# Kernel optimization log

Hardware: AMD Instinct MI355X
Metric: run time of the kernel (lower is better)

## Reference

```python
import jax, jax.numpy as jnp
import numpy as np

B, NW, L, D = 32, 64, 49, 192
HEADS, PROJ = 8, 256
HD = PROJ // HEADS  # 32


def setup_inputs() -> dict:
    key = jax.random.key(0)
    ks = jax.random.split(key, 12)
    s = 0.02
    return {
        "query": jax.random.normal(ks[0], (B, NW, L, D), jnp.float32),
        "key_": jax.random.normal(ks[1], (B, NW, L, D), jnp.float32),
        "value": jax.random.normal(ks[2], (B, NW, L, D), jnp.float32),
        "mask": jax.random.randint(ks[3], (1, NW, 1, L, L), 0, 2).astype(bool),
        "Wq": jax.random.normal(ks[4], (D, PROJ), jnp.float32) * s,
        "bq": jnp.zeros((PROJ,), jnp.float32),
        "Wk": jax.random.normal(ks[5], (D, PROJ), jnp.float32) * s,
        "bk": jnp.zeros((PROJ,), jnp.float32),
        "Wv": jax.random.normal(ks[6], (D, PROJ), jnp.float32) * s,
        "Ww": jax.random.normal(ks[7], (PROJ, D), jnp.float32) * s,
        "bw": jnp.zeros((D,), jnp.float32),
    }


def reference(query, key_, value, mask, Wq, bq, Wk, bk, Wv, Ww, bw):
    scale = 1.0 / (HD ** 0.5)
    # projections, split heads: [B, NW, L, PROJ] -> [B, NW, H, L, HD]
    def split_heads(x):
        return x.reshape(B, NW, L, HEADS, HD).transpose(0, 1, 3, 2, 4)

    q = split_heads(query @ Wq + bq)
    k = split_heads(key_ @ Wk + bk)
    v = split_heads(value @ Wv)  # no bias, matching proj_v

    # scores: [B, NW, H, L, L]
    scores = jnp.einsum("bwhnc,bwhmc->bwhnm", q, k) * scale
    scores = jnp.where(mask, jnp.float32(-1000.0), scores)
    attn = jax.nn.softmax(scores, axis=-1)
    # dropout inactive: training=False and enable_sampling=False

    out = jnp.einsum("bwhnm,bwhmc->bwhnc", attn, v)
    out = out.transpose(0, 1, 3, 2, 4).reshape(B, NW, L, PROJ)
    out = out @ Ww + bw
    return out
```

## Files before the change

### kernel.cpp

```cpp
#include <hip/hip_runtime.h>

#define B_    32
#define NW_   64
#define BW_   2048
#define L_    49
#define D_    192
#define PROJ_ 256
#define H_    8
#define HD_   32

typedef __attribute__((ext_vector_type(8))) short bf16x8;
typedef __attribute__((ext_vector_type(4))) float f32x4;

#define XB_OFF    0
#define QKP_OFF   25600
#define VT_OFF    91136
#define LDS_BYTES 123904

__device__ __forceinline__ short f2bf(float f) {
    union { float f; unsigned u; } v; v.f = f;
    unsigned r = v.u + 0x7FFFu + ((v.u >> 16) & 1u);
    return (short)(r >> 16);
}

__global__ __launch_bounds__(256) void prep_weights(
    const float* __restrict__ Wq, const float* __restrict__ Wk,
    const float* __restrict__ Wv, const float* __restrict__ Ww,
    short* __restrict__ Wqt, short* __restrict__ Wkt,
    short* __restrict__ Wvt, short* __restrict__ Wwt)
{
    const int sel = blockIdx.y;
    const int n   = blockIdx.x;
    const int tid = threadIdx.x;
    if (sel < 3) {
        const float* src = (sel == 0) ? Wq : (sel == 1) ? Wk : Wv;
        short* dst = (sel == 0) ? Wqt : (sel == 1) ? Wkt : Wvt;
        if (tid < D_) dst[n * D_ + tid] = f2bf(src[tid * PROJ_ + n]);
    } else {
        if (n < D_) Wwt[n * PROJ_ + tid] = f2bf(Ww[tid * D_ + n]);
    }
}

__global__ __launch_bounds__(256) void prep_mask(
    const int* __restrict__ mask, unsigned long long* __restrict__ mbits)
{
    const int w    = blockIdx.x;
    const int wave = threadIdx.x >> 6;
    const int lane = threadIdx.x & 63;
    for (int qq = 0; qq < 16; ++qq) {
        const int q = wave * 16 + qq;
        int val = 0;
        if (q < L_ && lane < L_) val = mask[w * (L_ * L_) + q * L_ + lane];
        unsigned long long bits = __ballot(val != 0);
        if (lane == 0) mbits[w * 64 + q] = bits;
    }
}

__global__ __launch_bounds__(512) void fused_kernel(
    const float* __restrict__ query, const float* __restrict__ key_,
    const float* __restrict__ value,
    const short* __restrict__ Wqt, const short* __restrict__ Wkt,
    const short* __restrict__ Wvt,
    const float* __restrict__ bq, const float* __restrict__ bk,
    const unsigned long long* __restrict__ mbits,
    const short* __restrict__ Wwt, const float* __restrict__ bwb,
    float* __restrict__ out)
{
    extern __shared__ char lds[];
    short* Xb = (short*)(lds + XB_OFF);

    const int bw   = blockIdx.x;
    const int w    = bw & (NW_ - 1);
    const int tid  = threadIdx.x;
    const int wave = tid >> 6;
    const int lane = tid & 63;
    const int m16  = lane & 15;
    const int quad = lane >> 4;

    const int swz2 = ((m16 >> 1) & 3) << 4;
    const int swz3 = (m16 & 7) << 4;

    char* myQKP = lds + QKP_OFF + wave * 8192;
    char* myVT  = lds + VT_OFF  + wave * 4096;

    #pragma unroll
    for (int sel = 0; sel < 3; ++sel) {
        const float* x  = (sel == 0) ? query : (sel == 1) ? key_ : value;
        const short* Wt = (sel == 0) ? Wqt : (sel == 1) ? Wkt : Wvt;

        __syncthreads();
        #pragma unroll
        for (int it = 0; it < 6; ++it) {
            const int i = tid + it * 512;
            const int l = i / 48, c4 = i - l * 48;
            short4 s4 = {0, 0, 0, 0};
            if (l < L_) {
                float4 v = *(const float4*)&x[((size_t)bw * L_ + l) * D_ + c4 * 4];
                s4.x = f2bf(v.x); s4.y = f2bf(v.y); s4.z = f2bf(v.z); s4.w = f2bf(v.w);
            }
            *(short4*)&Xb[l * 200 + c4 * 4] = s4;
        }
        __syncthreads();

        f32x4 acc[4][2];
        #pragma unroll
        for (int mt = 0; mt < 4; ++mt)
            #pragma unroll
            for (int nt = 0; nt < 2; ++nt)
                acc[mt][nt] = (f32x4){0.f, 0.f, 0.f, 0.f};

        #pragma unroll
        for (int kc = 0; kc < 6; ++kc) {
            bf16x8 af[4], bf[2];
            #pragma unroll
            for (int mt = 0; mt < 4; ++mt)
                af[mt] = *(const bf16x8*)&Xb[(mt * 16 + m16) * 200 + kc * 32 + quad * 8];
            #pragma unroll
            for (int nt = 0; nt < 2; ++nt)
                bf[nt] = *(const bf16x8*)&Wt[(size_t)(wave * 32 + nt * 16 + m16) * D_ + kc * 32 + quad * 8];
            #pragma unroll
            for (int mt = 0; mt < 4; ++mt)
                #pragma unroll
                for (int nt = 0; nt < 2; ++nt)
                    acc[mt][nt] = __builtin_amdgcn_mfma_f32_16x16x32_bf16(
                        af[mt], bf[nt], acc[mt][nt], 0, 0, 0);
        }

        if (sel < 2) {
            char* dstb = myQKP + sel * 4096;
            #pragma unroll
            for (int nt = 0; nt < 2; ++nt) {
                const int c = nt * 16 + m16;
                const float bias = ((sel == 0) ? bq : bk)[wave * 32 + c];
                #pragma unroll
                for (int mt = 0; mt < 4; ++mt)
                    #pragma unroll
                    for (int r = 0; r < 4; ++r) {
                        const int i = mt * 16 + quad * 4 + r;
                        *(short*)(dstb + i * 64 + ((2 * c) ^ (((i >> 1) & 3) << 4))) =
                            f2bf(acc[mt][nt][r] + bias);
                    }
            }
        } else {
            #pragma unroll
            for (int nt = 0; nt < 2; ++nt) {
                const int c = nt * 16 + m16;
                #pragma unroll
                for (int mt = 0; mt < 4; ++mt) {
                    short4 o4;
                    o4.x = f2bf(acc[mt][nt][0]); o4.y = f2bf(acc[mt][nt][1]);
                    o4.z = f2bf(acc[mt][nt][2]); o4.w = f2bf(acc[mt][nt][3]);
                    *(short4*)(myVT + c * 128 + ((mt * 32 + quad * 8) ^ swz3)) = o4;
                }
            }
        }
    }

    unsigned long long mb[4];
    #pragma unroll
    for (int nt = 0; nt < 4; ++nt) mb[nt] = mbits[w * 64 + nt * 16 + m16];

    const float scale = 0.17677669529663687f;

    f32x4 sacc[4][4];
    #pragma unroll
    for (int mt = 0; mt < 4; ++mt)
        #pragma unroll
        for (int nt = 0; nt < 4; ++nt)
            sacc[mt][nt] = (f32x4){0.f, 0.f, 0.f, 0.f};
    {
        bf16x8 kf[4], qf[4];
        #pragma unroll
        for (int mt = 0; mt < 4; ++mt)
            kf[mt] = *(const bf16x8*)(myQKP + 4096 + (mt * 16 + m16) * 64 + ((quad * 16) ^ swz2));
        #pragma unroll
        for (int nt = 0; nt < 4; ++nt)
            qf[nt] = *(const bf16x8*)(myQKP + (nt * 16 + m16) * 64 + ((quad * 16) ^ swz2));
        #pragma unroll
        for (int mt = 0; mt < 4; ++mt)
            #pragma unroll
            for (int nt = 0; nt < 4; ++nt)
                sacc[mt][nt] = __builtin_amdgcn_mfma_f32_16x16x32_bf16(
                    kf[mt], qf[nt], sacc[mt][nt], 0, 0, 0);
    }

    #pragma unroll
    for (int nt = 0; nt < 4; ++nt) {
        float e[4][4];
        float mx = -1e30f;
        #pragma unroll
        for (int mt = 0; mt < 4; ++mt)
            #pragma unroll
            for (int r = 0; r < 4; ++r) {
                const int k = mt * 16 + quad * 4 + r;
                float v = sacc[mt][nt][r] * scale;
                if (k >= L_) v = -INFINITY;
                else if ((mb[nt] >> k) & 1ull) v = -1000.0f;
                e[mt][r] = v;
                mx = fmaxf(mx, v);
            }
        mx = fmaxf(mx, __shfl_xor(mx, 16, 64));
        mx = fmaxf(mx, __shfl_xor(mx, 32, 64));
        float sum = 0.f;
        #pragma unroll
        for (int mt = 0; mt < 4; ++mt)
            #pragma unroll
            for (int r = 0; r < 4; ++r) {
                const float ev = __expf(e[mt][r] - mx);
                e[mt][r] = ev;
                sum += ev;
            }
        sum += __shfl_xor(sum, 16, 64);
        sum += __shfl_xor(sum, 32, 64);
        const float inv = 1.0f / sum;
        const int prow = nt * 16 + m16;
        #pragma unroll
        for (int mt = 0; mt < 4; ++mt) {
            short4 p4;
            p4.x = f2bf(e[mt][0] * inv); p4.y = f2bf(e[mt][1] * inv);
            p4.z = f2bf(e[mt][2] * inv); p4.w = f2bf(e[mt][3] * inv);
            *(short4*)(myQKP + prow * 128 + ((mt * 32 + quad * 8) ^ swz3)) = p4;
        }
    }

    f32x4 oacc[2][4];
    #pragma unroll
    for (int mt2 = 0; mt2 < 2; ++mt2)
        #pragma unroll
        for (int nt = 0; nt < 4; ++nt)
            oacc[mt2][nt] = (f32x4){0.f, 0.f, 0.f, 0.f};
    #pragma unroll
    for (int kc = 0; kc < 2; ++kc) {
        bf16x8 vf[2], pf[4];
        #pragma unroll
        for (int mt2 = 0; mt2 < 2; ++mt2)
            vf[mt2] = *(const bf16x8*)(myVT + (mt2 * 16 + m16) * 128 + ((kc * 64 + quad * 16) ^ swz3));
        #pragma unroll
        for (int nt = 0; nt < 4; ++nt)
            pf[nt] = *(const bf16x8*)(myQKP + (nt * 16 + m16) * 128 + ((kc * 64 + quad * 16) ^ swz3));
        #pragma unroll
        for (int mt2 = 0; mt2 < 2; ++mt2)
            #pragma unroll
            for (int nt = 0; nt < 4; ++nt)
                oacc[mt2][nt] = __builtin_amdgcn_mfma_f32_16x16x32_bf16(
                    vf[mt2], pf[nt], oacc[mt2][nt], 0, 0, 0);
    }

    #pragma unroll
    for (int nt = 0; nt < 4; ++nt) {
        const int prow = nt * 16 + m16;
        #pragma unroll
        for (int mt2 = 0; mt2 < 2; ++mt2) {
            short4 o4;
            o4.x = f2bf(oacc[mt2][nt][0]); o4.y = f2bf(oacc[mt2][nt][1]);
            o4.z = f2bf(oacc[mt2][nt][2]); o4.w = f2bf(oacc[mt2][nt][3]);
            *(short4*)(myQKP + prow * 64 + ((mt2 * 32 + quad * 8) ^ ((prow >> 1 & 3) << 4))) = o4;
        }
    }

    __syncthreads();

    f32x4 cacc[4][2];
    #pragma unroll
    for (int mt = 0; mt < 4; ++mt)
        #pragma unroll
        for (int nt = 0; nt < 2; ++nt)
            cacc[mt][nt] = (f32x4){0.f, 0.f, 0.f, 0.f};
    const int ntN = (wave < 4) ? 2 : 1;
    #pragma unroll
    for (int kc = 0; kc < 8; ++kc) {
        bf16x8 af[4], bfw[2];
        #pragma unroll
        for (int mt = 0; mt < 4; ++mt)
            af[mt] = *(const bf16x8*)(lds + QKP_OFF + kc * 8192 + (mt * 16 + m16) * 64 + ((quad * 16) ^ swz2));
        #pragma unroll
        for (int nt = 0; nt < 2; ++nt)
            if (nt < ntN) {
                const int tile = wave + nt * 8;
                bfw[nt] = *(const bf16x8*)&Wwt[(size_t)(tile * 16 + m16) * PROJ_ + kc * 32 + quad * 8];
            }
        #pragma unroll
        for (int mt = 0; mt < 4; ++mt)
            #pragma unroll
            for (int nt = 0; nt < 2; ++nt)
                if (nt < ntN)
                    cacc[mt][nt] = __builtin_amdgcn_mfma_f32_16x16x32_bf16(
                        af[mt], bfw[nt], cacc[mt][nt], 0, 0, 0);
    }
    #pragma unroll
    for (int nt = 0; nt < 2; ++nt) {
        if (nt < ntN) {
            const int col = (wave + nt * 8) * 16 + m16;
            const float bias = bwb[col];
            #pragma unroll
            for (int mt = 0; mt < 4; ++mt)
                #pragma unroll
                for (int r = 0; r < 4; ++r) {
                    const int i = mt * 16 + quad * 4 + r;
                    if (i < L_)
                        out[((size_t)bw * L_ + i) * D_ + col] = cacc[mt][nt][r] + bias;
                }
        }
    }
}

extern "C" void kernel_launch(void* const* d_in, const int* in_sizes, int n_in,
                              void* d_out, int out_size, void* d_ws, size_t ws_size,
                              hipStream_t stream) {
    const float* query = (const float*)d_in[0];
    const float* key_  = (const float*)d_in[1];
    const float* value = (const float*)d_in[2];
    const int*   mask  = (const int*)d_in[3];
    const float* Wq    = (const float*)d_in[4];
    const float* bq    = (const float*)d_in[5];
    const float* Wk    = (const float*)d_in[6];
    const float* bk    = (const float*)d_in[7];
    const float* Wv    = (const float*)d_in[8];
    const float* Ww    = (const float*)d_in[9];
    const float* bw    = (const float*)d_in[10];
    float* out = (float*)d_out;

    unsigned long long* mbits = (unsigned long long*)d_ws;
    short* Wqt = (short*)(mbits + 64 * 64);
    short* Wkt = Wqt + PROJ_ * D_;
    short* Wvt = Wkt + PROJ_ * D_;
    short* Wwt = Wvt + PROJ_ * D_;

    static bool attr_set = false;
    if (!attr_set) {
        (void)hipFuncSetAttribute(reinterpret_cast<const void*>(fused_kernel),
                                  hipFuncAttributeMaxDynamicSharedMemorySize, LDS_BYTES);
        attr_set = true;
    }

    prep_weights<<<dim3(256, 4), 256, 0, stream>>>(Wq, Wk, Wv, Ww, Wqt, Wkt, Wvt, Wwt);
    prep_mask<<<dim3(64), 256, 0, stream>>>(mask, mbits);
    fused_kernel<<<dim3(BW_), 512, LDS_BYTES, stream>>>(
        query, key_, value, Wqt, Wkt, Wvt, bq, bk, mbits, Wwt, bw, out);
}
```

Before: 403.0 us.

## Restructure fused attention to 4 waves with compact LDS for two blocks per CU

Halves the block to 256 threads, with each wave handling two heads. LDS shrinks from about 124KB to 79KB by packing Q/K per head only for the 49 valid rows and reusing the X buffer as per-wave V slots, so two blocks can fit per CU. The second head's V is kept in registers and spilled into the slot after the first head finishes. It also packs bf16 with v_cvt_pk_bf16_f32, adds s_setprio around MFMA bursts, and merges the two prep kernels into one launch. The cost is higher register pressure per wave and a serial two-head loop inside each wave.

```diff
diff --git a/kernel.cpp b/kernel.cpp
--- a/kernel.cpp
+++ b/kernel.cpp
@@ -12,10 +12,8 @@
 typedef __attribute__((ext_vector_type(8))) short bf16x8;
 typedef __attribute__((ext_vector_type(4))) float f32x4;
 
-#define XB_OFF    0
-#define QKP_OFF   25600
-#define VT_OFF    91136
-#define LDS_BYTES 123904
+#define QK_OFF    24576
+#define LDS_BYTES 78848
 
 __device__ __forceinline__ short f2bf(float f) {
     union { float f; unsigned u; } v; v.f = f;
@@ -23,40 +21,46 @@
     return (short)(r >> 16);
 }
 
-__global__ __launch_bounds__(256) void prep_weights(
+__device__ __forceinline__ unsigned cvtpk(float lo, float hi) {
+    unsigned r;
+    asm("v_cvt_pk_bf16_f32 %0, %1, %2" : "=v"(r) : "v"(lo), "v"(hi));
+    return r;
+}
+
+__global__ __launch_bounds__(256) void prep_kernel(
     const float* __restrict__ Wq, const float* __restrict__ Wk,
     const float* __restrict__ Wv, const float* __restrict__ Ww,
+    const int* __restrict__ mask,
     short* __restrict__ Wqt, short* __restrict__ Wkt,
-    short* __restrict__ Wvt, short* __restrict__ Wwt)
+    short* __restrict__ Wvt, short* __restrict__ Wwt,
+    unsigned long long* __restrict__ mbits)
 {
-    const int sel = blockIdx.y;
-    const int n   = blockIdx.x;
+    const int b   = blockIdx.x;
     const int tid = threadIdx.x;
-    if (sel < 3) {
+    if (b < 768) {
+        const int sel = b >> 8, n = b & 255;
         const float* src = (sel == 0) ? Wq : (sel == 1) ? Wk : Wv;
         short* dst = (sel == 0) ? Wqt : (sel == 1) ? Wkt : Wvt;
         if (tid < D_) dst[n * D_ + tid] = f2bf(src[tid * PROJ_ + n]);
+    } else if (b < 960) {
+        const int n = b - 768;
+        Wwt[n * PROJ_ + tid] = f2bf(Ww[tid * D_ + n]);
     } else {
-        if (n < D_) Wwt[n * PROJ_ + tid] = f2bf(Ww[tid * D_ + n]);
-    }
-}
-
-__global__ __launch_bounds__(256) void prep_mask(
-    const int* __restrict__ mask, unsigned long long* __restrict__ mbits)
-{
-    const int w    = blockIdx.x;
-    const int wave = threadIdx.x >> 6;
-    const int lane = threadIdx.x & 63;
-    for (int qq = 0; qq < 16; ++qq) {
-        const int q = wave * 16 + qq;
-        int val = 0;
-        if (q < L_ && lane < L_) val = mask[w * (L_ * L_) + q * L_ + lane];
-        unsigned long long bits = __ballot(val != 0);
-        if (lane == 0) mbits[w * 64 + q] = bits;
-    }
-}
-
-__global__ __launch_bounds__(512) void fused_kernel(
+        const int m = b - 960;
+        const int w = m >> 2, chunk = m & 3;
+        const int wave = tid >> 6, lane = tid & 63;
+        #pragma unroll
+        for (int k = 0; k < 4; ++k) {
+            const int q = chunk * 16 + wave * 4 + k;
+            int val = 0;
+            if (q < L_ && lane < L_) val = mask[w * (L_ * L_) + q * L_ + lane];
+            unsigned long long bits = __ballot(val != 0);
+            if (lane == 0) mbits[w * 64 + q] = bits;
+        }
+    }
+}
+
+__global__ __launch_bounds__(256, 2) void fused_kernel(
     const float* __restrict__ query, const float* __restrict__ key_,
     const float* __restrict__ value,
     const short* __restrict__ Wqt, const short* __restrict__ Wkt,
@@ -67,7 +71,6 @@
     float* __restrict__ out)
 {
     extern __shared__ char lds[];
-    short* Xb = (short*)(lds + XB_OFF);
 
     const int bw   = blockIdx.x;
     const int w    = bw & (NW_ - 1);
@@ -80,8 +83,14 @@
     const int swz2 = ((m16 >> 1) & 3) << 4;
     const int swz3 = (m16 & 7) << 4;
 
-    char* myQKP = lds + QKP_OFF + wave * 8192;
-    char* myVT  = lds + VT_OFF  + wave * 4096;
+    char* qkR  = lds + QK_OFF;
+    char* slot = lds + wave * 4096;
+
+    unsigned long long mb[4];
+    #pragma unroll
+    for (int nt = 0; nt < 4; ++nt) mb[nt] = mbits[w * 64 + nt * 16 + m16];
+
+    uint2 vpk[2][4];
 
     #pragma unroll
     for (int sel = 0; sel < 3; ++sel) {
@@ -90,217 +99,250 @@
 
         __syncthreads();
         #pragma unroll
-        for (int it = 0; it < 6; ++it) {
-            const int i = tid + it * 512;
+        for (int it = 0; it < 12; ++it) {
+            const int i = tid + it * 256;
             const int l = i / 48, c4 = i - l * 48;
-            short4 s4 = {0, 0, 0, 0};
+            uint2 u = {0u, 0u};
             if (l < L_) {
                 float4 v = *(const float4*)&x[((size_t)bw * L_ + l) * D_ + c4 * 4];
-                s4.x = f2bf(v.x); s4.y = f2bf(v.y); s4.z = f2bf(v.z); s4.w = f2bf(v.w);
-            }
-            *(short4*)&Xb[l * 200 + c4 * 4] = s4;
+                u.x = cvtpk(v.x, v.y); u.y = cvtpk(v.z, v.w);
+            }
+            *(uint2*)(lds + l * 384 + ((c4 * 8) ^ ((l & 7) << 4))) = u;
         }
         __syncthreads();
 
-        f32x4 acc[4][2];
-        #pragma unroll
-        for (int mt = 0; mt < 4; ++mt)
-            #pragma unroll
-            for (int nt = 0; nt < 2; ++nt)
+        f32x4 acc[4][4];
+        #pragma unroll
+        for (int mt = 0; mt < 4; ++mt)
+            #pragma unroll
+            for (int nt = 0; nt < 4; ++nt)
                 acc[mt][nt] = (f32x4){0.f, 0.f, 0.f, 0.f};
 
         #pragma unroll
         for (int kc = 0; kc < 6; ++kc) {
-            bf16x8 af[4], bf[2];
-            #pragma unroll
-            for (int mt = 0; mt < 4; ++mt)
-                af[mt] = *(const bf16x8*)&Xb[(mt * 16 + m16) * 200 + kc * 32 + quad * 8];
-            #pragma unroll
-            for (int nt = 0; nt < 2; ++nt)
-                bf[nt] = *(const bf16x8*)&Wt[(size_t)(wave * 32 + nt * 16 + m16) * D_ + kc * 32 + quad * 8];
-            #pragma unroll
-            for (int mt = 0; mt < 4; ++mt)
-                #pragma unroll
-                for (int nt = 0; nt < 2; ++nt)
+            bf16x8 af[4], bfr[4];
+            #pragma unroll
+            for (int mt = 0; mt < 4; ++mt)
+                af[mt] = *(const bf16x8*)(lds + (mt * 16 + m16) * 384 +
+                                          ((kc * 64 + quad * 16) ^ swz3));
+            #pragma unroll
+            for (int nt = 0; nt < 4; ++nt)
+                bfr[nt] = *(const bf16x8*)&Wt[(size_t)(wave * 64 + nt * 16 + m16) * D_ +
+                                              kc * 32 + quad * 8];
+            __builtin_amdgcn_s_setprio(1);
+            #pragma unroll
+            for (int mt = 0; mt < 4; ++mt)
+                #pragma unroll
+                for (int nt = 0; nt < 4; ++nt)
                     acc[mt][nt] = __builtin_amdgcn_mfma_f32_16x16x32_bf16(
-                        af[mt], bf[nt], acc[mt][nt], 0, 0, 0);
-        }
+                        af[mt], bfr[nt], acc[mt][nt], 0, 0, 0);
+            __builtin_amdgcn_s_setprio(0);
+        }
+
+        if (sel == 2) __syncthreads();
 
         if (sel < 2) {
-            char* dstb = myQKP + sel * 4096;
-            #pragma unroll
-            for (int nt = 0; nt < 2; ++nt) {
-                const int c = nt * 16 + m16;
-                const float bias = ((sel == 0) ? bq : bk)[wave * 32 + c];
+            const float* bsel = (sel == 0) ? bq : bk;
+            #pragma unroll
+            for (int nt = 0; nt < 4; ++nt) {
+                const int head = wave * 2 + (nt >> 1);
+                const int c = (nt & 1) * 16 + m16;
+                const float bias = bsel[wave * 64 + nt * 16 + m16];
+                char* db = qkR + head * 6272 + sel * 3136;
                 #pragma unroll
                 for (int mt = 0; mt < 4; ++mt)
                     #pragma unroll
                     for (int r = 0; r < 4; ++r) {
                         const int i = mt * 16 + quad * 4 + r;
-                        *(short*)(dstb + i * 64 + ((2 * c) ^ (((i >> 1) & 3) << 4))) =
-                            f2bf(acc[mt][nt][r] + bias);
+                        if (i < L_)
+                            *(short*)(db + i * 64 + ((2 * c) ^ (((i >> 1) & 3) << 4))) =
+                                f2bf(acc[mt][nt][r] + bias);
                     }
             }
         } else {
             #pragma unroll
-            for (int nt = 0; nt < 2; ++nt) {
-                const int c = nt * 16 + m16;
+            for (int nt = 0; nt < 4; ++nt) {
+                const int c = (nt & 1) * 16 + m16;
                 #pragma unroll
                 for (int mt = 0; mt < 4; ++mt) {
-                    short4 o4;
-                    o4.x = f2bf(acc[mt][nt][0]); o4.y = f2bf(acc[mt][nt][1]);
-                    o4.z = f2bf(acc[mt][nt][2]); o4.w = f2bf(acc[mt][nt][3]);
-                    *(short4*)(myVT + c * 128 + ((mt * 32 + quad * 8) ^ swz3)) = o4;
-                }
-            }
-        }
-    }
-
-    unsigned long long mb[4];
-    #pragma unroll
-    for (int nt = 0; nt < 4; ++nt) mb[nt] = mbits[w * 64 + nt * 16 + m16];
+                    uint2 p;
+                    p.x = cvtpk(acc[mt][nt][0], acc[mt][nt][1]);
+                    p.y = cvtpk(acc[mt][nt][2], acc[mt][nt][3]);
+                    if (nt < 2)
+                        *(uint2*)(slot + c * 128 + ((mt * 32 + quad * 8) ^ swz3)) = p;
+                    else
+                        vpk[nt - 2][mt] = p;
+                }
+            }
+        }
+    }
 
     const float scale = 0.17677669529663687f;
 
-    f32x4 sacc[4][4];
+    #pragma unroll 1
+    for (int hh = 0; hh < 2; ++hh) {
+        const int head = wave * 2 + hh;
+        char* qb = qkR + head * 6272;
+        char* kb = qb + 3136;
+
+        f32x4 sacc[4][4];
+        #pragma unroll
+        for (int mt = 0; mt < 4; ++mt)
+            #pragma unroll
+            for (int nt = 0; nt < 4; ++nt)
+                sacc[mt][nt] = (f32x4){0.f, 0.f, 0.f, 0.f};
+        {
+            bf16x8 kf[4], qf[4];
+            #pragma unroll
+            for (int mt = 0; mt < 4; ++mt)
+                kf[mt] = *(const bf16x8*)(kb + (mt * 16 + m16) * 64 + ((quad * 16) ^ swz2));
+            #pragma unroll
+            for (int nt = 0; nt < 4; ++nt)
+                qf[nt] = *(const bf16x8*)(qb + (nt * 16 + m16) * 64 + ((quad * 16) ^ swz2));
+            __builtin_amdgcn_s_setprio(1);
+            #pragma unroll
+            for (int mt = 0; mt < 4; ++mt)
+                #pragma unroll
+                for (int nt = 0; nt < 4; ++nt)
+                    sacc[mt][nt] = __builtin_amdgcn_mfma_f32_16x16x32_bf16(
+                        kf[mt], qf[nt], sacc[mt][nt], 0, 0, 0);
+            __builtin_amdgcn_s_setprio(0);
+        }
+
+        #pragma unroll
+        for (int nt = 0; nt < 4; ++nt) {
+            float e[4][4];
+            float mx = -1e30f;
+            #pragma unroll
+            for (int mt = 0; mt < 4; ++mt)
+                #pragma unroll
+                for (int r = 0; r < 4; ++r) {
+                    const int k = mt * 16 + quad * 4 + r;
+                    float v = sacc[mt][nt][r] * scale;
+                    if (k >= L_) v = -INFINITY;
+                    else if ((mb[nt] >> k) & 1ull) v = -1000.0f;
+                    e[mt][r] = v;
+                    mx = fmaxf(mx, v);
+                }
+            mx = fmaxf(mx, __shfl_xor(mx, 16, 64));
+            mx = fmaxf(mx, __shfl_xor(mx, 32, 64));
+            float sum = 0.f;
+            #pragma unroll
+            for (int mt = 0; mt < 4; ++mt)
+                #pragma unroll
+                for (int r = 0; r < 4; ++r) {
+                    const float ev = __expf(e[mt][r] - mx);
+                    e[mt][r] = ev;
+                    sum += ev;
+                }
+            sum += __shfl_xor(sum, 16, 64);
+            sum += __shfl_xor(sum, 32, 64);
+            const float inv = 1.0f / sum;
+            const int prow = nt * 16 + m16;
+            if (prow < L_) {
+                #pragma unroll
+                for (int mt = 0; mt < 4; ++mt) {
+                    uint2 p;
+                    p.x = cvtpk(e[mt][0] * inv, e[mt][1] * inv);
+                    p.y = cvtpk(e[mt][2] * inv, e[mt][3] * inv);
+                    *(uint2*)(qb + prow * 128 + ((mt * 32 + quad * 8) ^ swz3)) = p;
+                }
+            }
+        }
+
+        f32x4 oacc[2][4];
+        #pragma unroll
+        for (int mt2 = 0; mt2 < 2; ++mt2)
+            #pragma unroll
+            for (int nt = 0; nt < 4; ++nt)
+                oacc[mt2][nt] = (f32x4){0.f, 0.f, 0.f, 0.f};
+        #pragma unroll
+        for (int kc = 0; kc < 2; ++kc) {
+            bf16x8 vf[2], pf[4];
+            #pragma unroll
+            for (int mt2 = 0; mt2 < 2; ++mt2)
+                vf[mt2] = *(const bf16x8*)(slot + (mt2 * 16 + m16) * 128 +
+                                           ((kc * 64 + quad * 16) ^ swz3));
+            #pragma unroll
+            for (int nt = 0; nt < 4; ++nt)
+                pf[nt] = *(const bf16x8*)(qb + (nt * 16 + m16) * 128 +
+                                          ((kc * 64 + quad * 16) ^ swz3));
+            __builtin_amdgcn_s_setprio(1);
+            #pragma unroll
+            for (int mt2 = 0; mt2 < 2; ++mt2)
+                #pragma unroll
+                for (int nt = 0; nt < 4; ++nt)
+                    oacc[mt2][nt] = __builtin_amdgcn_mfma_f32_16x16x32_bf16(
+                        vf[mt2], pf[nt], oacc[mt2][nt], 0, 0, 0);
+            __builtin_amdgcn_s_setprio(0);
+        }
+
+        #pragma unroll
+        for (int nt = 0; nt < 4; ++nt) {
+            const int prow = nt * 16 + m16;
+            if (prow < L_) {
+                #pragma unroll
+                for (int mt2 = 0; mt2 < 2; ++mt2) {
+                    uint2 o;
+                    o.x = cvtpk(oacc[mt2][nt][0], oacc[mt2][nt][1]);
+                    o.y = cvtpk(oacc[mt2][nt][2], oacc[mt2][nt][3]);
+                    *(uint2*)(qb + prow * 64 +
+                              ((mt2 * 32 + quad * 8) ^ (((prow >> 1) & 3) << 4))) = o;
+                }
+            }
+        }
+
+        if (hh == 0) {
+            #pragma unroll
+            for (int nt2 = 0; nt2 < 2; ++nt2) {
+                const int c = nt2 * 16 + m16;
+                #pragma unroll
+                for (int mt = 0; mt < 4; ++mt)
+                    *(uint2*)(slot + c * 128 + ((mt * 32 + quad * 8) ^ swz3)) = vpk[nt2][mt];
+            }
+        }
+    }
+
+    __syncthreads();
+
+    f32x4 cacc[4][3];
     #pragma unroll
     for (int mt = 0; mt < 4; ++mt)
         #pragma unroll
-        for (int nt = 0; nt < 4; ++nt)
-            sacc[mt][nt] = (f32x4){0.f, 0.f, 0.f, 0.f};
-    {
-        bf16x8 kf[4], qf[4];
-        #pragma unroll
-        for (int mt = 0; mt < 4; ++mt)
-            kf[mt] = *(const bf16x8*)(myQKP + 4096 + (mt * 16 + m16) * 64 + ((quad * 16) ^ swz2));
-        #pragma unroll
-        for (int nt = 0; nt < 4; ++nt)
-            qf[nt] = *(const bf16x8*)(myQKP + (nt * 16 + m16) * 64 + ((quad * 16) ^ swz2));
-        #pragma unroll
-        for (int mt = 0; mt < 4; ++mt)
-            #pragma unroll
-            for (int nt = 0; nt < 4; ++nt)
-                sacc[mt][nt] = __builtin_amdgcn_mfma_f32_16x16x32_bf16(
-                    kf[mt], qf[nt], sacc[mt][nt], 0, 0, 0);
-    }
-
-    #pragma unroll
-    for (int nt = 0; nt < 4; ++nt) {
-        float e[4][4];
-        float mx = -1e30f;
+        for (int nt = 0; nt < 3; ++nt)
+            cacc[mt][nt] = (f32x4){0.f, 0.f, 0.f, 0.f};
+    #pragma unroll
+    for (int kc = 0; kc < 8; ++kc) {
+        char* Oh = qkR + kc * 6272;
+        bf16x8 af[4], bfw[3];
+        #pragma unroll
+        for (int mt = 0; mt < 4; ++mt)
+            af[mt] = *(const bf16x8*)(Oh + (mt * 16 + m16) * 64 + ((quad * 16) ^ swz2));
+        #pragma unroll
+        for (int nt = 0; nt < 3; ++nt)
+            bfw[nt] = *(const bf16x8*)&Wwt[(size_t)(wave * 48 + nt * 16 + m16) * PROJ_ +
+                                           kc * 32 + quad * 8];
+        __builtin_amdgcn_s_setprio(1);
+        #pragma unroll
+        for (int mt = 0; mt < 4; ++mt)
+            #pragma unroll
+            for (int nt = 0; nt < 3; ++nt)
+                cacc[mt][nt] = __builtin_amdgcn_mfma_f32_16x16x32_bf16(
+                    af[mt], bfw[nt], cacc[mt][nt], 0, 0, 0);
+        __builtin_amdgcn_s_setprio(0);
+    }
+    #pragma unroll
+    for (int nt = 0; nt < 3; ++nt) {
+        const int col = wave * 48 + nt * 16 + m16;
+        const float bias = bwb[col];
         #pragma unroll
         for (int mt = 0; mt < 4; ++mt)
             #pragma unroll
             for (int r = 0; r < 4; ++r) {
-                const int k = mt * 16 + quad * 4 + r;
-                float v = sacc[mt][nt][r] * scale;
-                if (k >= L_) v = -INFINITY;
-                else if ((mb[nt] >> k) & 1ull) v = -1000.0f;
-                e[mt][r] = v;
-                mx = fmaxf(mx, v);
-            }
-        mx = fmaxf(mx, __shfl_xor(mx, 16, 64));
-        mx = fmaxf(mx, __shfl_xor(mx, 32, 64));
-        float sum = 0.f;
-        #pragma unroll
-        for (int mt = 0; mt < 4; ++mt)
-            #pragma unroll
-            for (int r = 0; r < 4; ++r) {
-                const float ev = __expf(e[mt][r] - mx);
-                e[mt][r] = ev;
-                sum += ev;
-            }
-        sum += __shfl_xor(sum, 16, 64);
-        sum += __shfl_xor(sum, 32, 64);
-        const float inv = 1.0f / sum;
-        const int prow = nt * 16 + m16;
-        #pragma unroll
-        for (int mt = 0; mt < 4; ++mt) {
-            short4 p4;
-            p4.x = f2bf(e[mt][0] * inv); p4.y = f2bf(e[mt][1] * inv);
-            p4.z = f2bf(e[mt][2] * inv); p4.w = f2bf(e[mt][3] * inv);
-            *(short4*)(myQKP + prow * 128 + ((mt * 32 + quad * 8) ^ swz3)) = p4;
-        }
-    }
-
-    f32x4 oacc[2][4];
-    #pragma unroll
-    for (int mt2 = 0; mt2 < 2; ++mt2)
-        #pragma unroll
-        for (int nt = 0; nt < 4; ++nt)
-            oacc[mt2][nt] = (f32x4){0.f, 0.f, 0.f, 0.f};
-    #pragma unroll
-    for (int kc = 0; kc < 2; ++kc) {
-        bf16x8 vf[2], pf[4];
-        #pragma unroll
-        for (int mt2 = 0; mt2 < 2; ++mt2)
-            vf[mt2] = *(const bf16x8*)(myVT + (mt2 * 16 + m16) * 128 + ((kc * 64 + quad * 16) ^ swz3));
-        #pragma unroll
-        for (int nt = 0; nt < 4; ++nt)
-            pf[nt] = *(const bf16x8*)(myQKP + (nt * 16 + m16) * 128 + ((kc * 64 + quad * 16) ^ swz3));
-        #pragma unroll
-        for (int mt2 = 0; mt2 < 2; ++mt2)
-            #pragma unroll
-            for (int nt = 0; nt < 4; ++nt)
-                oacc[mt2][nt] = __builtin_amdgcn_mfma_f32_16x16x32_bf16(
-                    vf[mt2], pf[nt], oacc[mt2][nt], 0, 0, 0);
-    }
-
-    #pragma unroll
-    for (int nt = 0; nt < 4; ++nt) {
-        const int prow = nt * 16 + m16;
-        #pragma unroll
-        for (int mt2 = 0; mt2 < 2; ++mt2) {
-            short4 o4;
-            o4.x = f2bf(oacc[mt2][nt][0]); o4.y = f2bf(oacc[mt2][nt][1]);
-            o4.z = f2bf(oacc[mt2][nt][2]); o4.w = f2bf(oacc[mt2][nt][3]);
-            *(short4*)(myQKP + prow * 64 + ((mt2 * 32 + quad * 8) ^ ((prow >> 1 & 3) << 4))) = o4;
-        }
-    }
-
-    __syncthreads();
-
-    f32x4 cacc[4][2];
-    #pragma unroll
-    for (int mt = 0; mt < 4; ++mt)
-        #pragma unroll
-        for (int nt = 0; nt < 2; ++nt)
-            cacc[mt][nt] = (f32x4){0.f, 0.f, 0.f, 0.f};
-    const int ntN = (wave < 4) ? 2 : 1;
-    #pragma unroll
-    for (int kc = 0; kc < 8; ++kc) {
-        bf16x8 af[4], bfw[2];
-        #pragma unroll
-        for (int mt = 0; mt < 4; ++mt)
-            af[mt] = *(const bf16x8*)(lds + QKP_OFF + kc * 8192 + (mt * 16 + m16) * 64 + ((quad * 16) ^ swz2));
-        #pragma unroll
-        for (int nt = 0; nt < 2; ++nt)
-            if (nt < ntN) {
-                const int tile = wave + nt * 8;
-                bfw[nt] = *(const bf16x8*)&Wwt[(size_t)(tile * 16 + m16) * PROJ_ + kc * 32 + quad * 8];
-            }
-        #pragma unroll
-        for (int mt = 0; mt < 4; ++mt)
-            #pragma unroll
-            for (int nt = 0; nt < 2; ++nt)
-                if (nt < ntN)
-                    cacc[mt][nt] = __builtin_amdgcn_mfma_f32_16x16x32_bf16(
-                        af[mt], bfw[nt], cacc[mt][nt], 0, 0, 0);
-    }
-    #pragma unroll
-    for (int nt = 0; nt < 2; ++nt) {
-        if (nt < ntN) {
-            const int col = (wave + nt * 8) * 16 + m16;
-            const float bias = bwb[col];
-            #pragma unroll
-            for (int mt = 0; mt < 4; ++mt)
-                #pragma unroll
-                for (int r = 0; r < 4; ++r) {
-                    const int i = mt * 16 + quad * 4 + r;
-                    if (i < L_)
-                        out[((size_t)bw * L_ + i) * D_ + col] = cacc[mt][nt][r] + bias;
-                }
-        }
+                const int i = mt * 16 + quad * 4 + r;
+                if (i < L_)
+                    out[((size_t)bw * L_ + i) * D_ + col] = cacc[mt][nt][r] + bias;
+            }
     }
 }
 
@@ -333,8 +375,8 @@
         attr_set = true;
     }
 
-    prep_weights<<<dim3(256, 4), 256, 0, stream>>>(Wq, Wk, Wv, Ww, Wqt, Wkt, Wvt, Wwt);
-    prep_mask<<<dim3(64), 256, 0, stream>>>(mask, mbits);
-    fused_kernel<<<dim3(BW_), 512, LDS_BYTES, stream>>>(
+    prep_kernel<<<dim3(1216), 256, 0, stream>>>(Wq, Wk, Wv, Ww, mask,
+                                                Wqt, Wkt, Wvt, Wwt, mbits);
+    fused_kernel<<<dim3(BW_), 256, LDS_BYTES, stream>>>(
         query, key_, value, Wqt, Wkt, Wvt, bq, bk, mbits, Wwt, bw, out);
 }
```

Result: faster. 367.0 us (-8.9%).
